# Performance work log

Measured on AMD Instinct MI355X. Metric: run time of the kernel, lower is better.

## Reference

```python
import jax, jax.numpy as jnp
import numpy as np
from jax import lax

B, T, F = 64, 100, 128
HD = [32, 64]            # encoder hidden dims; decoder uses reversed [64, 32]
KH, KW = 3, 3


def _conv(x, w):
    # x: (b, cin, f, 1), w: (cout, cin, kh, kw), SAME padding
    ph, pw = w.shape[2] // 2, w.shape[3] // 2
    return lax.conv_general_dilated(x, w, (1, 1), [(ph, ph), (pw, pw)],
                                    dimension_numbers=("NCHW", "OIHW", "NCHW"))


def _run_layer(xs, h0, wg, bg, wc, bc):
    # xs: (t, b, cin, f, 1); h0: (b, hd, f, 1)
    def step(h, x):
        g = _conv(jnp.concatenate([x, h], axis=1), wg) + bg[None, :, None, None]
        r, u = jnp.split(jax.nn.sigmoid(g), 2, axis=1)
        c = jnp.tanh(_conv(jnp.concatenate([x, r * h], axis=1), wc) + bc[None, :, None, None])
        h_next = (1.0 - u) * h + u * c
        return h_next, h_next
    h_last, ys = lax.scan(step, h0, xs)
    return ys, h_last


def setup_inputs() -> dict:
    key = jax.random.key(0)
    ks = iter(jax.random.split(key, 32))
    s = 0.05
    d = {"x": jax.random.normal(next(ks), (B, T, F), dtype=jnp.float32)}
    # encoder: layer0 in=1 hd=32, layer1 in=32 hd=64
    # decoder: input_dim=64, hidden reversed [64,32]: layer0 in=64 hd=64, layer1 in=64 hd=32
    specs = {
        "e0": (1, 32), "e1": (32, 64),
        "d0": (64, 64), "d1": (64, 32),
    }
    for name, (cin, hd) in specs.items():
        d[name + "_wg"] = jax.random.normal(next(ks), (2 * hd, cin + hd, KH, KW), dtype=jnp.float32) * s
        d[name + "_bg"] = jnp.zeros((2 * hd,), dtype=jnp.float32)
        d[name + "_wc"] = jax.random.normal(next(ks), (hd, cin + hd, KH, KW), dtype=jnp.float32) * s
        d[name + "_bc"] = jnp.zeros((hd,), dtype=jnp.float32)
    d["fw"] = jax.random.normal(next(ks), (1, 32, 1, 1), dtype=jnp.float32) * s
    d["fb"] = jnp.zeros((1,), dtype=jnp.float32)
    return d


def reference(x,
              e0_wg, e0_bg, e0_wc, e0_bc,
              e1_wg, e1_bg, e1_wc, e1_bc,
              d0_wg, d0_bg, d0_wc, d0_bc,
              d1_wg, d1_bg, d1_wc, d1_bc,
              fw, fb):
    b, t, f = x.shape
    xs = x.reshape(b, t, 1, f, 1).transpose(1, 0, 2, 3, 4)  # (t,b,1,f,1)
    zeros = lambda hd: jnp.zeros((b, hd, f, 1), dtype=x.dtype)
    # encoder (return_all_layers; decoder consumes last layer output)
    y0, h0 = _run_layer(xs, zeros(HD[0]), e0_wg, e0_bg, e0_wc, e0_bc)
    y1, h1 = _run_layer(y0, zeros(HD[1]), e1_wg, e1_bg, e1_wc, e1_bc)
    # decoder init states = encoder last states reversed: [h1 (64ch), h0 (32ch)]
    z0, _ = _run_layer(y1, h1, d0_wg, d0_bg, d0_wc, d0_bc)
    z1, _ = _run_layer(z0, h0, d1_wg, d1_bg, d1_wc, d1_bc)
    # final 1x1 conv: (t,b,32,f,1) x (1,32) -> (t,b,1,f,1)
    rec = jnp.einsum("tbcfw,oc->tbofw", z1, fw[:, :, 0, 0]) + fb[None, None, :, None, None]
    return rec.transpose(1, 0, 2, 3, 4).reshape(b, t, f)
```

## Files before the change

kernel.cpp:

```cpp
#include <hip/hip_runtime.h>
#include <cstdint>
#include <cstddef>


#define F_ 128
#define T_ 100
#define B_ 64
#define ROWSP 130
#define CBSTR (ROWSP * 8)
#define CBBYTE (ROWSP * 16)
#define AT_OFF 104448
#define LDS_TOTAL (AT_OFF + 28 * CBBYTE)

typedef _Float16 f16;
typedef __attribute__((ext_vector_type(4))) float f32x4;
typedef __attribute__((ext_vector_type(8))) _Float16 f16x8;
typedef __attribute__((ext_vector_type(4))) _Float16 f16x4;

#define MFMA(a, b, c) __builtin_amdgcn_mfma_f32_16x16x32_f16(a, b, c, 0, 0, 0)

__device__ __forceinline__ float exp2_(float x) { return __builtin_amdgcn_exp2f(x); }
__device__ __forceinline__ float rcp_(float x) { return __builtin_amdgcn_rcpf(x); }

#define KSG (-1.442695041f)
#define KTH (-2.885390082f)

__host__ __device__ constexpr int cbA(int lid, int km) {
  return lid == 0 ? (km ? 4 : 0)
       : lid == 1 ? (1 + km * 4)
       : lid == 2 ? (km * 4)
                  : (8 + km * 4);
}
__host__ __device__ constexpr int cbB(int lid, int km) {
  return lid == 0 ? (km ? 17 : 13)
       : lid == 1 ? (km == 0 ? 1 : 14 + km * 4)
       : lid == 2 ? (km < 2 ? km * 4 : 12 + km * 4)
                  : (km < 2 ? 8 + km * 4 : 20);
}

template <int LID, int NCR, int NK, int NC3, int HC, int RHC, bool GREG, bool EMITY1>
__device__ __forceinline__ void gru_layer(
    const f16* __restrict__ rdB, char* __restrict__ wrB,
    const f16x8* __restrict__ aR, const f16x8* __restrict__ aU,
    const f16* __restrict__ gR, const f16* __restrict__ gU,
    const f16* __restrict__ cW, const f32x4 bR2, const f32x4 bU2,
    const f32x4 bC2, f32x4* __restrict__ hreg, f16* __restrict__ y1dst) {
  constexpr int FTW = NCR;
  f32x4 accR[FTW], accU[FTW];
#pragma unroll
  for (int j = 0; j < FTW; ++j) {
    accR[j] = (f32x4){0.f, 0.f, 0.f, 0.f};
    accU[j] = (f32x4){0.f, 0.f, 0.f, 0.f};
  }
#pragma unroll
  for (int ks = 0; ks < NK; ++ks) {
    const int k = ks / NC3, km = ks % NC3;
    const f16* fb = rdB + cbA(LID, km) * CBSTR + k * 8;
    f16x8 bf[FTW];
#pragma unroll
    for (int j = 0; j < FTW; ++j) bf[j] = *(const f16x8*)(fb + j * 128);
    f16x8 wr, wu;
    if constexpr (GREG) {
      wr = aR[ks];
      wu = aU[ks];
    } else {
      wr = *(const f16x8*)(gR + ks * 512);
      wu = *(const f16x8*)(gU + ks * 512);
    }
#pragma unroll
    for (int j = 0; j < FTW; ++j) accR[j] = MFMA(wr, bf[j], accR[j]);
#pragma unroll
    for (int j = 0; j < FTW; ++j) accU[j] = MFMA(wu, bf[j], accU[j]);
  }
#pragma unroll
  for (int j = 0; j < FTW; ++j) {
    f16x4 rh;
#pragma unroll
    for (int q = 0; q < 4; ++q) {
      const float r = rcp_(1.0f + exp2_(fmaf(accR[j][q], KSG, bR2[q])));
      rh[q] = (f16)(r * hreg[j][q]);
    }
    *(f16x4*)(wrB + (RHC >> 3) * CBBYTE + j * 256) = rh;
  }
  __syncthreads();
  f32x4 accC[FTW];
#pragma unroll
  for (int j = 0; j < FTW; ++j) accC[j] = (f32x4){0.f, 0.f, 0.f, 0.f};
#pragma unroll
  for (int ks = 0; ks < NK; ++ks) {
    const int k = ks / NC3, km = ks % NC3;
    const f16* fb = rdB + cbB(LID, km) * CBSTR + k * 8;
    f16x8 bf[FTW];
#pragma unroll
    for (int j = 0; j < FTW; ++j) bf[j] = *(const f16x8*)(fb + j * 128);
    const f16x8 wc = *(const f16x8*)(cW + ks * 512);
#pragma unroll
    for (int j = 0; j < FTW; ++j) accC[j] = MFMA(wc, bf[j], accC[j]);
  }
#pragma unroll
  for (int j = 0; j < FTW; ++j) {
    f16x4 hh;
#pragma unroll
    for (int q = 0; q < 4; ++q) {
      const float u = rcp_(1.0f + exp2_(fmaf(accU[j][q], KSG, bU2[q])));
      const float r = rcp_(1.0f + exp2_(fmaf(accC[j][q], KTH, bC2[q])));
      const float h = hreg[j][q];
      const float s = fmaf(2.0f, r, -(1.0f + h));
      const float hn = fmaf(u, s, h);
      hreg[j][q] = hn;
      hh[q] = (f16)hn;
    }
    *(f16x4*)(wrB + (HC >> 3) * CBBYTE + j * 256) = hh;
    if constexpr (EMITY1) *(f16x4*)(y1dst + j * 128) = hh;
  }
}

__global__ __launch_bounds__(512, 2) void ae_kernel(
    const f16* __restrict__ xf, float* __restrict__ out,
    const f16* __restrict__ wgE0, const f16* __restrict__ wcE0,
    const float* __restrict__ bgE0, const float* __restrict__ bcE0,
    const f16* __restrict__ wgE1, const f16* __restrict__ wcE1,
    const float* __restrict__ bgE1, const float* __restrict__ bcE1,
    const f16* __restrict__ wgD0, const f16* __restrict__ wcD0,
    const float* __restrict__ bgD0, const float* __restrict__ bcD0,
    const f16* __restrict__ wgD1, const f16* __restrict__ wcD1,
    const float* __restrict__ bgD1, const float* __restrict__ bcD1,
    const float* __restrict__ fw, const float* __restrict__ fb,
    f16* __restrict__ y1g) {
  extern __shared__ char smem[];
  f16* aT = (f16*)(smem + AT_OFF);
  const int tid = threadIdx.x, b = blockIdx.x;
  const int w = tid >> 6, l = tid & 63;
  const int m16 = l & 15, kb = l >> 4;

  for (int i = tid; i < 28 * CBBYTE / 16; i += 512)
    ((f32x4*)(smem + AT_OFF))[i] = (f32x4){0.f, 0.f, 0.f, 0.f};
  for (int i = tid; i < 1536; i += 512)
    ((f16x8*)(smem + 0))[i] = ((const f16x8*)wgE0)[i];
  for (int i = tid; i < 768; i += 512)
    ((f16x8*)(smem + 24576))[i] = ((const f16x8*)wcE0)[i];
  for (int i = tid; i < 2304; i += 512)
    ((f16x8*)(smem + 36864))[i] = ((const f16x8*)wcE1)[i];

  const int cot2 = w & 1, cot4 = w & 3;
  f16x8 aR1[9], aU1[9];
#pragma unroll
  for (int ks = 0; ks < 9; ++ks) {
    aR1[ks] = ((const f16x8*)wgE1)[(cot4 * 9 + ks) * 64 + l];
    aU1[ks] = ((const f16x8*)wgE1)[((cot4 + 4) * 9 + ks) * 64 + l];
  }
  const int co2 = cot2 * 16 + kb * 4;
  const int co4 = cot4 * 16 + kb * 4;
  f32x4 bRe0, bUe0, bCe0, bRe1, bUe1, bCe1;
#pragma unroll
  for (int q = 0; q < 4; ++q) {
    bRe0[q] = bgE0[co2 + q] * KSG;
    bUe0[q] = bgE0[32 + co2 + q] * KSG;
    bCe0[q] = bcE0[co2 + q] * KTH;
    bRe1[q] = bgE1[co4 + q] * KSG;
    bUe1[q] = bgE1[64 + co4 + q] * KSG;
    bCe1[q] = bcE1[co4 + q] * KTH;
  }
  const int ft2 = (w >> 1) * 2, ft4 = (w >> 2) * 4;
  const f16* rdB2 = aT + kb * CBSTR + (ft2 * 16 + m16) * 8;
  const f16* rdB4 = aT + kb * CBSTR + (ft4 * 16 + m16) * 8;
  char* wrB2 = (char*)aT + (cot2 * 2 + (kb >> 1)) * CBBYTE +
               (ft2 * 16 + m16 + 1) * 16 + (kb & 1) * 8;
  char* wrB4 = (char*)aT + (cot4 * 2 + (kb >> 1)) * CBBYTE +
               (ft4 * 16 + m16 + 1) * 16 + (kb & 1) * 8;
  f16* y1t = y1g + (size_t)b * T_ * 8192 +
             ((cot4 * 2 + (kb >> 1)) * 128 + ft4 * 16 + m16) * 8 + (kb & 1) * 4;
  const f16* gE0R = (const f16*)(smem + 0) + (cot2 * 6 * 64 + l) * 8;
  const f16* gE0U = (const f16*)(smem + 0) + ((cot2 + 2) * 6 * 64 + l) * 8;
  const f16* cE0 = (const f16*)(smem + 24576) + (cot2 * 6 * 64 + l) * 8;
  const f16* cE1 = (const f16*)(smem + 36864) + (cot4 * 9 * 64 + l) * 8;

  f32x4 h0r[2], h1r[4];
#pragma unroll
  for (int j = 0; j < 2; ++j) h0r[j] = (f32x4){0.f, 0.f, 0.f, 0.f};
#pragma unroll
  for (int j = 0; j < 4; ++j) h1r[j] = (f32x4){0.f, 0.f, 0.f, 0.f};
  __syncthreads();

  const f16* xb = xf + (size_t)b * T_ * F_;
  for (int t = 0; t < T_; ++t) {
    if (tid < F_) {
      const f16 v = xb[t * F_ + tid];
      aT[(tid + 1) * 8] = v;
      aT[13 * CBSTR + (tid + 1) * 8] = v;
    }
    __syncthreads();
    gru_layer<0, 2, 6, 2, 8, 112, false, false>(
        rdB2, wrB2, nullptr, nullptr, gE0R, gE0U, cE0, bRe0, bUe0, bCe0, h0r,
        nullptr);
    __syncthreads();
    gru_layer<1, 4, 9, 3, 40, 144, true, true>(
        rdB4, wrB4, aR1, aU1, nullptr, nullptr, cE1, bRe1, bUe1, bCe1, h1r,
        y1t + t * 8192);
    __syncthreads();
  }

  {
#pragma unroll
    for (int j = 0; j < 4; ++j) {
      f16x4 hh;
#pragma unroll
      for (int q = 0; q < 4; ++q) hh[q] = (f16)h1r[j][q];
      *(f16x4*)(wrB4 + 8 * CBBYTE + j * 256) = hh;
    }
#pragma unroll
    for (int j = 0; j < 2; ++j) {
      f16x4 hh;
#pragma unroll
      for (int q = 0; q < 4; ++q) hh[q] = (f16)h0r[j][q];
      *(f16x4*)(wrB2 + 16 * CBBYTE + j * 256) = hh;
    }
  }
  for (int i = tid; i < 3072; i += 512)
    ((f16x8*)(smem + 0))[i] = ((const f16x8*)wcD0)[i];
  for (int i = tid; i < 2304; i += 512)
    ((f16x8*)(smem + 49152))[i] = ((const f16x8*)wgD1)[i];
  for (int i = tid; i < 1152; i += 512)
    ((f16x8*)(smem + 86016))[i] = ((const f16x8*)wcD1)[i];
  f16x8 aR0[12], aU0[12];
#pragma unroll
  for (int ks = 0; ks < 12; ++ks) {
    aR0[ks] = ((const f16x8*)wgD0)[(cot4 * 12 + ks) * 64 + l];
    aU0[ks] = ((const f16x8*)wgD0)[((cot4 + 4) * 12 + ks) * 64 + l];
  }
  f32x4 bRd0, bUd0, bCd0, bRd1, bUd1, bCd1;
#pragma unroll
  for (int q = 0; q < 4; ++q) {
    bRd0[q] = bgD0[co4 + q] * KSG;
    bUd0[q] = bgD0[64 + co4 + q] * KSG;
    bCd0[q] = bcD0[co4 + q] * KTH;
    bRd1[q] = bgD1[co2 + q] * KSG;
    bUd1[q] = bgD1[32 + co2 + q] * KSG;
    bCd1[q] = bcD1[co2 + q] * KTH;
  }
  const f16* gD1R = (const f16*)(smem + 49152) + (cot2 * 9 * 64 + l) * 8;
  const f16* gD1U = (const f16*)(smem + 49152) + ((cot2 + 2) * 9 * 64 + l) * 8;
  const f16* cD0 = (const f16*)(smem + 0) + (cot4 * 12 * 64 + l) * 8;
  const f16* cD1 = (const f16*)(smem + 86016) + (cot2 * 9 * 64 + l) * 8;
  __syncthreads();

  for (int t = 0; t < T_; ++t) {
    {
      const f16x8* src = (const f16x8*)(y1g + ((size_t)b * T_ + t) * 8192);
#pragma unroll
      for (int k2 = 0; k2 < 2; ++k2) {
        const int i = tid + k2 * 512;
        *(f16x8*)&aT[(i >> 7) * CBSTR + ((i & 127) + 1) * 8] = src[i];
      }
    }
    __syncthreads();
    gru_layer<2, 4, 12, 4, 64, 160, true, false>(
        rdB4, wrB4, aR0, aU0, nullptr, nullptr, cD0, bRd0, bUd0, bCd0, h1r,
        nullptr);
    __syncthreads();
    gru_layer<3, 2, 9, 3, 128, 160, false, false>(
        rdB2, wrB2, nullptr, nullptr, gD1R, gD1U, cD1, bRd1, bUd1, bCd1, h0r,
        nullptr);
    __syncthreads();
    if (tid < F_) {
      float s = fb[0];
#pragma unroll
      for (int cb = 0; cb < 4; ++cb) {
        const f16x8 h8 = *(const f16x8*)&aT[(16 + cb) * CBSTR + (tid + 1) * 8];
#pragma unroll
        for (int q = 0; q < 8; ++q) s = fmaf(fw[cb * 8 + q], (float)h8[q], s);
      }
      out[((size_t)b * T_ + t) * F_ + tid] = s;
    }
  }
}

__global__ void repack_f16(const float* __restrict__ src, f16* __restrict__ dst,
                           int CO, int CI, int CINH, int NK, int e0map) {
  const int n = (CO / 16) * NK * 64;
  for (int i = blockIdx.x * blockDim.x + threadIdx.x; i < n;
       i += gridDim.x * blockDim.x) {
    const int cot = i / (NK * 64);
    const int r = i - cot * NK * 64;
    const int ks = r >> 6, lph = r & 63;
    const int co = cot * 16 + (lph & 15);
    const int kbl = lph >> 4;
#pragma unroll
    for (int j = 0; j < 8; ++j) {
      const int kk = ks * 32 + kbl * 8 + j;
      const int k = kk / CINH, c = kk - k * CINH;
      int ci;
      if (e0map) ci = (c == 0) ? 0 : ((c >= 8 && c < 40) ? c - 7 : -1);
      else ci = (c < CI) ? c : -1;
      float wv = 0.f;
      if (ci >= 0) wv = src[((size_t)(co * CI + ci) * 3 + k) * 3 + 1];
      dst[(size_t)i * 8 + j] = (f16)wv;
    }
  }
}

__global__ void xcvt(const float* __restrict__ x, f16* __restrict__ xf, int n4) {
  for (int i = blockIdx.x * blockDim.x + threadIdx.x; i < n4;
       i += gridDim.x * blockDim.x) {
    const float4 v = ((const float4*)x)[i];
    f16x4 o;
    o[0] = (f16)v.x; o[1] = (f16)v.y; o[2] = (f16)v.z; o[3] = (f16)v.w;
    ((f16x4*)xf)[i] = o;
  }
}

extern "C" void kernel_launch(void* const* d_in, const int* in_sizes, int n_in,
                              void* d_out, int out_size, void* d_ws, size_t ws_size,
                              hipStream_t stream) {
  (void)in_sizes; (void)n_in; (void)out_size; (void)ws_size;
  const float* x = (const float*)d_in[0];
  const float* e0_wg = (const float*)d_in[1];
  const float* e0_bg = (const float*)d_in[2];
  const float* e0_wc = (const float*)d_in[3];
  const float* e0_bc = (const float*)d_in[4];
  const float* e1_wg = (const float*)d_in[5];
  const float* e1_bg = (const float*)d_in[6];
  const float* e1_wc = (const float*)d_in[7];
  const float* e1_bc = (const float*)d_in[8];
  const float* d0_wg = (const float*)d_in[9];
  const float* d0_bg = (const float*)d_in[10];
  const float* d0_wc = (const float*)d_in[11];
  const float* d0_bc = (const float*)d_in[12];
  const float* d1_wg = (const float*)d_in[13];
  const float* d1_bg = (const float*)d_in[14];
  const float* d1_wc = (const float*)d_in[15];
  const float* d1_bc = (const float*)d_in[16];
  const float* fw = (const float*)d_in[17];
  const float* fb = (const float*)d_in[18];
  float* out = (float*)d_out;

  char* p = (char*)d_ws;
  f16* y1g = (f16*)p;
  p += (size_t)B_ * T_ * 64 * 128 * 2;
  f16* xf = (f16*)p;
  p += (size_t)B_ * T_ * F_ * 2;
  auto aw = [&](int n) { f16* q = (f16*)p; p += (size_t)n * 2; return q; };
  f16* wgE0 = aw(64 * 192);
  f16* wcE0 = aw(32 * 192);
  f16* wgE1 = aw(128 * 288);
  f16* wcE1 = aw(64 * 288);
  f16* wgD0 = aw(128 * 384);
  f16* wcD0 = aw(64 * 384);
  f16* wgD1 = aw(64 * 288);
  f16* wcD1 = aw(32 * 288);

  auto rp = [&](const float* s, f16* d, int CO, int CI, int CINH, int e0m) {
    const int NK = 3 * CINH / 32;
    const int n = (CO / 16) * NK * 64;
    hipLaunchKernelGGL(repack_f16, dim3((n + 255) / 256), dim3(256), 0, stream,
                       s, d, CO, CI, CINH, NK, e0m);
  };
  rp(e0_wg, wgE0, 64, 33, 64, 1);
  rp(e0_wc, wcE0, 32, 33, 64, 1);
  rp(e1_wg, wgE1, 128, 96, 96, 0);
  rp(e1_wc, wcE1, 64, 96, 96, 0);
  rp(d0_wg, wgD0, 128, 128, 128, 0);
  rp(d0_wc, wcD0, 64, 128, 128, 0);
  rp(d1_wg, wgD1, 64, 96, 96, 0);
  rp(d1_wc, wcD1, 32, 96, 96, 0);
  hipLaunchKernelGGL(xcvt, dim3(200), dim3(1024), 0, stream, x, xf,
                     B_ * T_ * F_ / 4);

  hipFuncSetAttribute((const void*)ae_kernel,
                      hipFuncAttributeMaxDynamicSharedMemorySize, LDS_TOTAL);
  hipLaunchKernelGGL(ae_kernel, dim3(B_), dim3(512), LDS_TOTAL, stream, xf, out,
                     wgE0, wcE0, e0_bg, e0_bc, wgE1, wcE1, e1_bg, e1_bc,
                     wgD0, wcD0, d0_bg, d0_bc, wgD1, wcD1, d1_bg, d1_bc,
                     fw, fb, y1g);
}
```

Before: 1.272 ms.

## Retile GRU layers so each wave covers 32 features and multiple output tiles

Each wave now owns a fixed 32-feature slab (two column tiles) and one or two output-channel tiles, replacing the old split of 2 or 4 feature tiles per wave. One B-fragment load is then reused across all output tiles a wave computes. Weight placement is redistributed: some gate weights move to LDS, candidate weights for the encoder move into registers, and decoder candidate weights are read straight from global memory. The update-gate sigmoid is computed earlier, alongside the reset gate, before the barrier. This changes register pressure and adds global weight loads inside the decoder loop, which could stall on memory latency.

```diff
diff --git a/kernel.cpp b/kernel.cpp
--- a/kernel.cpp
+++ b/kernel.cpp
@@ -9,7 +9,7 @@
 #define ROWSP 130
 #define CBSTR (ROWSP * 8)
 #define CBBYTE (ROWSP * 16)
-#define AT_OFF 104448
+#define AT_OFF 100352
 #define LDS_TOTAL (AT_OFF + 28 * CBBYTE)
 
 typedef _Float16 f16;
@@ -38,80 +38,102 @@
                   : (km < 2 ? 8 + km * 4 : 20);
 }
 
-template <int LID, int NCR, int NK, int NC3, int HC, int RHC, bool GREG, bool EMITY1>
+template <int LID, int COT, int NK, int NC3, int HCB, int RHCB,
+          bool GREG, bool CGLOB, bool EMITY1>
 __device__ __forceinline__ void gru_layer(
     const f16* __restrict__ rdB, char* __restrict__ wrB,
-    const f16x8* __restrict__ aR, const f16x8* __restrict__ aU,
     const f16* __restrict__ gR, const f16* __restrict__ gU,
-    const f16* __restrict__ cW, const f32x4 bR2, const f32x4 bU2,
-    const f32x4 bC2, f32x4* __restrict__ hreg, f16* __restrict__ y1dst) {
-  constexpr int FTW = NCR;
-  f32x4 accR[FTW], accU[FTW];
-#pragma unroll
-  for (int j = 0; j < FTW; ++j) {
-    accR[j] = (f32x4){0.f, 0.f, 0.f, 0.f};
-    accU[j] = (f32x4){0.f, 0.f, 0.f, 0.f};
-  }
+    const f16x8* __restrict__ aRr, const f16x8* __restrict__ aUr,
+    const f16x8* __restrict__ cRr, const f16* __restrict__ cGb,
+    const f32x4 bR0, const f32x4 bR1, const f32x4 bU0, const f32x4 bU1,
+    const f32x4 bC0, const f32x4 bC1,
+    f32x4* __restrict__ hreg, f16* __restrict__ y1dst) {
+  f32x4 accR[COT][2], accU[COT][2];
+#pragma unroll
+  for (int i = 0; i < COT; ++i)
+#pragma unroll
+    for (int j = 0; j < 2; ++j) {
+      accR[i][j] = (f32x4){0.f, 0.f, 0.f, 0.f};
+      accU[i][j] = (f32x4){0.f, 0.f, 0.f, 0.f};
+    }
 #pragma unroll
   for (int ks = 0; ks < NK; ++ks) {
     const int k = ks / NC3, km = ks % NC3;
     const f16* fb = rdB + cbA(LID, km) * CBSTR + k * 8;
-    f16x8 bf[FTW];
-#pragma unroll
-    for (int j = 0; j < FTW; ++j) bf[j] = *(const f16x8*)(fb + j * 128);
-    f16x8 wr, wu;
-    if constexpr (GREG) {
-      wr = aR[ks];
-      wu = aU[ks];
-    } else {
-      wr = *(const f16x8*)(gR + ks * 512);
-      wu = *(const f16x8*)(gU + ks * 512);
-    }
-#pragma unroll
-    for (int j = 0; j < FTW; ++j) accR[j] = MFMA(wr, bf[j], accR[j]);
-#pragma unroll
-    for (int j = 0; j < FTW; ++j) accU[j] = MFMA(wu, bf[j], accU[j]);
-  }
-#pragma unroll
-  for (int j = 0; j < FTW; ++j) {
-    f16x4 rh;
-#pragma unroll
-    for (int q = 0; q < 4; ++q) {
-      const float r = rcp_(1.0f + exp2_(fmaf(accR[j][q], KSG, bR2[q])));
-      rh[q] = (f16)(r * hreg[j][q]);
-    }
-    *(f16x4*)(wrB + (RHC >> 3) * CBBYTE + j * 256) = rh;
+    const f16x8 b0 = *(const f16x8*)(fb);
+    const f16x8 b1 = *(const f16x8*)(fb + 128);
+#pragma unroll
+    for (int i = 0; i < COT; ++i) {
+      f16x8 wr, wu;
+      if constexpr (GREG) {
+        wr = aRr[i * NK + ks];
+        wu = aUr[i * NK + ks];
+      } else {
+        wr = *(const f16x8*)(gR + (i * NK + ks) * 512);
+        wu = *(const f16x8*)(gU + (i * NK + ks) * 512);
+      }
+      accR[i][0] = MFMA(wr, b0, accR[i][0]);
+      accR[i][1] = MFMA(wr, b1, accR[i][1]);
+      accU[i][0] = MFMA(wu, b0, accU[i][0]);
+      accU[i][1] = MFMA(wu, b1, accU[i][1]);
+    }
+  }
+  f32x4 u[COT][2];
+#pragma unroll
+  for (int i = 0; i < COT; ++i) {
+    const f32x4 bR = i ? bR1 : bR0;
+    const f32x4 bU = i ? bU1 : bU0;
+#pragma unroll
+    for (int j = 0; j < 2; ++j) {
+      f16x4 rh;
+#pragma unroll
+      for (int q = 0; q < 4; ++q) {
+        u[i][j][q] = rcp_(1.0f + exp2_(fmaf(accU[i][j][q], KSG, bU[q])));
+        const float r = rcp_(1.0f + exp2_(fmaf(accR[i][j][q], KSG, bR[q])));
+        rh[q] = (f16)(r * hreg[i * 2 + j][q]);
+      }
+      *(f16x4*)(wrB + (RHCB - HCB) * CBBYTE + i * 2 * CBBYTE + j * 256) = rh;
+    }
   }
   __syncthreads();
-  f32x4 accC[FTW];
-#pragma unroll
-  for (int j = 0; j < FTW; ++j) accC[j] = (f32x4){0.f, 0.f, 0.f, 0.f};
+  f32x4 accC[COT][2];
+#pragma unroll
+  for (int i = 0; i < COT; ++i)
+#pragma unroll
+    for (int j = 0; j < 2; ++j) accC[i][j] = (f32x4){0.f, 0.f, 0.f, 0.f};
 #pragma unroll
   for (int ks = 0; ks < NK; ++ks) {
     const int k = ks / NC3, km = ks % NC3;
     const f16* fb = rdB + cbB(LID, km) * CBSTR + k * 8;
-    f16x8 bf[FTW];
-#pragma unroll
-    for (int j = 0; j < FTW; ++j) bf[j] = *(const f16x8*)(fb + j * 128);
-    const f16x8 wc = *(const f16x8*)(cW + ks * 512);
-#pragma unroll
-    for (int j = 0; j < FTW; ++j) accC[j] = MFMA(wc, bf[j], accC[j]);
-  }
-#pragma unroll
-  for (int j = 0; j < FTW; ++j) {
-    f16x4 hh;
-#pragma unroll
-    for (int q = 0; q < 4; ++q) {
-      const float u = rcp_(1.0f + exp2_(fmaf(accU[j][q], KSG, bU2[q])));
-      const float r = rcp_(1.0f + exp2_(fmaf(accC[j][q], KTH, bC2[q])));
-      const float h = hreg[j][q];
-      const float s = fmaf(2.0f, r, -(1.0f + h));
-      const float hn = fmaf(u, s, h);
-      hreg[j][q] = hn;
-      hh[q] = (f16)hn;
-    }
-    *(f16x4*)(wrB + (HC >> 3) * CBBYTE + j * 256) = hh;
-    if constexpr (EMITY1) *(f16x4*)(y1dst + j * 128) = hh;
+    const f16x8 b0 = *(const f16x8*)(fb);
+    const f16x8 b1 = *(const f16x8*)(fb + 128);
+#pragma unroll
+    for (int i = 0; i < COT; ++i) {
+      f16x8 wc;
+      if constexpr (CGLOB) wc = *(const f16x8*)(cGb + (i * NK + ks) * 512);
+      else wc = cRr[i * NK + ks];
+      accC[i][0] = MFMA(wc, b0, accC[i][0]);
+      accC[i][1] = MFMA(wc, b1, accC[i][1]);
+    }
+  }
+#pragma unroll
+  for (int i = 0; i < COT; ++i) {
+    const f32x4 bC = i ? bC1 : bC0;
+#pragma unroll
+    for (int j = 0; j < 2; ++j) {
+      f16x4 hh;
+#pragma unroll
+      for (int q = 0; q < 4; ++q) {
+        const float r = rcp_(1.0f + exp2_(fmaf(accC[i][j][q], KTH, bC[q])));
+        const float h = hreg[i * 2 + j][q];
+        const float s = fmaf(2.0f, r, -(1.0f + h));
+        const float hn = fmaf(u[i][j][q], s, h);
+        hreg[i * 2 + j][q] = hn;
+        hh[q] = (f16)hn;
+      }
+      *(f16x4*)(wrB + i * 2 * CBBYTE + j * 256) = hh;
+      if constexpr (EMITY1) *(f16x4*)(y1dst + i * 2048 + j * 128) = hh;
+    }
   }
 }
 
@@ -129,51 +151,57 @@
     f16* __restrict__ y1g) {
   extern __shared__ char smem[];
   f16* aT = (f16*)(smem + AT_OFF);
+  char* atB = smem + AT_OFF;
   const int tid = threadIdx.x, b = blockIdx.x;
   const int w = tid >> 6, l = tid & 63;
-  const int m16 = l & 15, kb = l >> 4;
+  const int m16 = l & 15, kb = l >> 4, kb4 = kb * 4;
+  const int cg = w & 1, fg = w >> 1;
 
   for (int i = tid; i < 28 * CBBYTE / 16; i += 512)
-    ((f32x4*)(smem + AT_OFF))[i] = (f32x4){0.f, 0.f, 0.f, 0.f};
+    ((f32x4*)atB)[i] = (f32x4){0.f, 0.f, 0.f, 0.f};
+  for (int i = tid; i < 4608; i += 512)
+    ((f16x8*)smem)[i] = ((const f16x8*)wgE1)[i];
   for (int i = tid; i < 1536; i += 512)
-    ((f16x8*)(smem + 0))[i] = ((const f16x8*)wgE0)[i];
-  for (int i = tid; i < 768; i += 512)
-    ((f16x8*)(smem + 24576))[i] = ((const f16x8*)wcE0)[i];
-  for (int i = tid; i < 2304; i += 512)
-    ((f16x8*)(smem + 36864))[i] = ((const f16x8*)wcE1)[i];
-
-  const int cot2 = w & 1, cot4 = w & 3;
-  f16x8 aR1[9], aU1[9];
-#pragma unroll
-  for (int ks = 0; ks < 9; ++ks) {
-    aR1[ks] = ((const f16x8*)wgE1)[(cot4 * 9 + ks) * 64 + l];
-    aU1[ks] = ((const f16x8*)wgE1)[((cot4 + 4) * 9 + ks) * 64 + l];
-  }
-  const int co2 = cot2 * 16 + kb * 4;
-  const int co4 = cot4 * 16 + kb * 4;
-  f32x4 bRe0, bUe0, bCe0, bRe1, bUe1, bCe1;
+    ((f16x8*)(smem + 73728))[i] = ((const f16x8*)wgE0)[i];
+
+  f16x8 cE0[6], cE1[18];
+#pragma unroll
+  for (int ks = 0; ks < 6; ++ks)
+    cE0[ks] = ((const f16x8*)wcE0)[(cg * 6 + ks) * 64 + l];
+#pragma unroll
+  for (int i = 0; i < 2; ++i)
+#pragma unroll
+    for (int ks = 0; ks < 9; ++ks)
+      cE1[i * 9 + ks] = ((const f16x8*)wcE1)[((2 * cg + i) * 9 + ks) * 64 + l];
+
+  const int co2 = cg * 16 + kb4;
+  const int coA = (2 * cg) * 16 + kb4, coB = (2 * cg + 1) * 16 + kb4;
+  f32x4 bRe0, bUe0, bCe0, bRe1a, bRe1b, bUe1a, bUe1b, bCe1a, bCe1b;
 #pragma unroll
   for (int q = 0; q < 4; ++q) {
     bRe0[q] = bgE0[co2 + q] * KSG;
     bUe0[q] = bgE0[32 + co2 + q] * KSG;
     bCe0[q] = bcE0[co2 + q] * KTH;
-    bRe1[q] = bgE1[co4 + q] * KSG;
-    bUe1[q] = bgE1[64 + co4 + q] * KSG;
-    bCe1[q] = bcE1[co4 + q] * KTH;
-  }
-  const int ft2 = (w >> 1) * 2, ft4 = (w >> 2) * 4;
-  const f16* rdB2 = aT + kb * CBSTR + (ft2 * 16 + m16) * 8;
-  const f16* rdB4 = aT + kb * CBSTR + (ft4 * 16 + m16) * 8;
-  char* wrB2 = (char*)aT + (cot2 * 2 + (kb >> 1)) * CBBYTE +
-               (ft2 * 16 + m16 + 1) * 16 + (kb & 1) * 8;
-  char* wrB4 = (char*)aT + (cot4 * 2 + (kb >> 1)) * CBBYTE +
-               (ft4 * 16 + m16 + 1) * 16 + (kb & 1) * 8;
+    bRe1a[q] = bgE1[coA + q] * KSG;
+    bRe1b[q] = bgE1[coB + q] * KSG;
+    bUe1a[q] = bgE1[64 + coA + q] * KSG;
+    bUe1b[q] = bgE1[64 + coB + q] * KSG;
+    bCe1a[q] = bcE1[coA + q] * KTH;
+    bCe1b[q] = bcE1[coB + q] * KTH;
+  }
+
+  const f16* rdB = aT + kb * CBSTR + (fg * 32 + m16) * 8;
+  const int rowb = (fg * 32 + m16 + 1) * 16 + (kb & 1) * 8;
+  char* wrE0 = atB + (1 + cg * 2 + (kb >> 1)) * CBBYTE + rowb;
+  char* wrE1 = atB + (5 + 4 * cg + (kb >> 1)) * CBBYTE + rowb;
+  char* wrD0 = atB + (8 + 4 * cg + (kb >> 1)) * CBBYTE + rowb;
+  char* wrD1 = atB + (16 + cg * 2 + (kb >> 1)) * CBBYTE + rowb;
+  const f16* gRe1 = (const f16*)smem + (2 * cg * 9) * 512 + l * 8;
+  const f16* gUe1 = (const f16*)smem + ((4 + 2 * cg) * 9) * 512 + l * 8;
+  const f16* gRe0 = (const f16*)(smem + 73728) + (cg * 6) * 512 + l * 8;
+  const f16* gUe0 = (const f16*)(smem + 73728) + ((2 + cg) * 6) * 512 + l * 8;
   f16* y1t = y1g + (size_t)b * T_ * 8192 +
-             ((cot4 * 2 + (kb >> 1)) * 128 + ft4 * 16 + m16) * 8 + (kb & 1) * 4;
-  const f16* gE0R = (const f16*)(smem + 0) + (cot2 * 6 * 64 + l) * 8;
-  const f16* gE0U = (const f16*)(smem + 0) + ((cot2 + 2) * 6 * 64 + l) * 8;
-  const f16* cE0 = (const f16*)(smem + 24576) + (cot2 * 6 * 64 + l) * 8;
-  const f16* cE1 = (const f16*)(smem + 36864) + (cot4 * 9 * 64 + l) * 8;
+             ((4 * cg + (kb >> 1)) * 128 + fg * 32 + m16) * 8 + (kb & 1) * 4;
 
   f32x4 h0r[2], h1r[4];
 #pragma unroll
@@ -190,58 +218,59 @@
       aT[13 * CBSTR + (tid + 1) * 8] = v;
     }
     __syncthreads();
-    gru_layer<0, 2, 6, 2, 8, 112, false, false>(
-        rdB2, wrB2, nullptr, nullptr, gE0R, gE0U, cE0, bRe0, bUe0, bCe0, h0r,
-        nullptr);
-    __syncthreads();
-    gru_layer<1, 4, 9, 3, 40, 144, true, true>(
-        rdB4, wrB4, aR1, aU1, nullptr, nullptr, cE1, bRe1, bUe1, bCe1, h1r,
-        y1t + t * 8192);
+    gru_layer<0, 1, 6, 2, 1, 14, false, false, false>(
+        rdB, wrE0, gRe0, gUe0, nullptr, nullptr, cE0, nullptr,
+        bRe0, bRe0, bUe0, bUe0, bCe0, bCe0, h0r, nullptr);
+    __syncthreads();
+    gru_layer<1, 2, 9, 3, 5, 18, false, false, true>(
+        rdB, wrE1, gRe1, gUe1, nullptr, nullptr, cE1, nullptr,
+        bRe1a, bRe1b, bUe1a, bUe1b, bCe1a, bCe1b, h1r, y1t + t * 8192);
     __syncthreads();
   }
 
   {
 #pragma unroll
-    for (int j = 0; j < 4; ++j) {
-      f16x4 hh;
-#pragma unroll
-      for (int q = 0; q < 4; ++q) hh[q] = (f16)h1r[j][q];
-      *(f16x4*)(wrB4 + 8 * CBBYTE + j * 256) = hh;
-    }
+    for (int i = 0; i < 2; ++i)
+#pragma unroll
+      for (int j = 0; j < 2; ++j) {
+        f16x4 hh;
+#pragma unroll
+        for (int q = 0; q < 4; ++q) hh[q] = (f16)h1r[i * 2 + j][q];
+        *(f16x4*)(wrD0 + i * 2 * CBBYTE + j * 256) = hh;
+      }
 #pragma unroll
     for (int j = 0; j < 2; ++j) {
       f16x4 hh;
 #pragma unroll
       for (int q = 0; q < 4; ++q) hh[q] = (f16)h0r[j][q];
-      *(f16x4*)(wrB2 + 16 * CBBYTE + j * 256) = hh;
-    }
-  }
-  for (int i = tid; i < 3072; i += 512)
-    ((f16x8*)(smem + 0))[i] = ((const f16x8*)wcD0)[i];
-  for (int i = tid; i < 2304; i += 512)
-    ((f16x8*)(smem + 49152))[i] = ((const f16x8*)wgD1)[i];
-  for (int i = tid; i < 1152; i += 512)
-    ((f16x8*)(smem + 86016))[i] = ((const f16x8*)wcD1)[i];
-  f16x8 aR0[12], aU0[12];
-#pragma unroll
-  for (int ks = 0; ks < 12; ++ks) {
-    aR0[ks] = ((const f16x8*)wgD0)[(cot4 * 12 + ks) * 64 + l];
-    aU0[ks] = ((const f16x8*)wgD0)[((cot4 + 4) * 12 + ks) * 64 + l];
-  }
-  f32x4 bRd0, bUd0, bCd0, bRd1, bUd1, bCd1;
+      *(f16x4*)(wrD1 + j * 256) = hh;
+    }
+  }
+  for (int i = tid; i < 6144; i += 512)
+    ((f16x8*)smem)[i] = ((const f16x8*)wgD0)[i];
+  f16x8 aRd1[9], aUd1[9];
+#pragma unroll
+  for (int ks = 0; ks < 9; ++ks) {
+    aRd1[ks] = ((const f16x8*)wgD1)[(cg * 9 + ks) * 64 + l];
+    aUd1[ks] = ((const f16x8*)wgD1)[((2 + cg) * 9 + ks) * 64 + l];
+  }
+  f32x4 bRd0a, bRd0b, bUd0a, bUd0b, bCd0a, bCd0b, bRd1, bUd1, bCd1;
 #pragma unroll
   for (int q = 0; q < 4; ++q) {
-    bRd0[q] = bgD0[co4 + q] * KSG;
-    bUd0[q] = bgD0[64 + co4 + q] * KSG;
-    bCd0[q] = bcD0[co4 + q] * KTH;
+    bRd0a[q] = bgD0[coA + q] * KSG;
+    bRd0b[q] = bgD0[coB + q] * KSG;
+    bUd0a[q] = bgD0[64 + coA + q] * KSG;
+    bUd0b[q] = bgD0[64 + coB + q] * KSG;
+    bCd0a[q] = bcD0[coA + q] * KTH;
+    bCd0b[q] = bcD0[coB + q] * KTH;
     bRd1[q] = bgD1[co2 + q] * KSG;
     bUd1[q] = bgD1[32 + co2 + q] * KSG;
     bCd1[q] = bcD1[co2 + q] * KTH;
   }
-  const f16* gD1R = (const f16*)(smem + 49152) + (cot2 * 9 * 64 + l) * 8;
-  const f16* gD1U = (const f16*)(smem + 49152) + ((cot2 + 2) * 9 * 64 + l) * 8;
-  const f16* cD0 = (const f16*)(smem + 0) + (cot4 * 12 * 64 + l) * 8;
-  const f16* cD1 = (const f16*)(smem + 86016) + (cot2 * 9 * 64 + l) * 8;
+  const f16* gRd0 = (const f16*)smem + (2 * cg * 12) * 512 + l * 8;
+  const f16* gUd0 = (const f16*)smem + ((4 + 2 * cg) * 12) * 512 + l * 8;
+  const f16* cGd0 = (const f16*)wcD0 + (2 * cg * 12) * 512 + l * 8;
+  const f16* cGd1 = (const f16*)wcD1 + (cg * 9) * 512 + l * 8;
   __syncthreads();
 
   for (int t = 0; t < T_; ++t) {
@@ -254,13 +283,13 @@
       }
     }
     __syncthreads();
-    gru_layer<2, 4, 12, 4, 64, 160, true, false>(
-        rdB4, wrB4, aR0, aU0, nullptr, nullptr, cD0, bRd0, bUd0, bCd0, h1r,
-        nullptr);
-    __syncthreads();
-    gru_layer<3, 2, 9, 3, 128, 160, false, false>(
-        rdB2, wrB2, nullptr, nullptr, gD1R, gD1U, cD1, bRd1, bUd1, bCd1, h0r,
-        nullptr);
+    gru_layer<2, 2, 12, 4, 8, 20, false, true, false>(
+        rdB, wrD0, gRd0, gUd0, nullptr, nullptr, nullptr, cGd0,
+        bRd0a, bRd0b, bUd0a, bUd0b, bCd0a, bCd0b, h1r, nullptr);
+    __syncthreads();
+    gru_layer<3, 1, 9, 3, 16, 20, true, true, false>(
+        rdB, wrD1, nullptr, nullptr, aRd1, aUd1, nullptr, cGd1,
+        bRd1, bRd1, bUd1, bUd1, bCd1, bCd1, h0r, nullptr);
     __syncthreads();
     if (tid < F_) {
       float s = fb[0];
```

New measurement: 1.566 ms. 23.1% more time.
